# Kernel optimization log

Measured on AMD Instinct MI355X. Metric: run time of the kernel, lower is better.

Reference implementation:

```python
import jax, jax.numpy as jnp
import numpy as np

CROP_H = 7
CROP_W = 7
EXTRAP = 0.0  # module hardcodes 0 when calling CropAndResizeFunction


def _crop_and_resize(image, boxes, box_ind):
    """TF-style crop_and_resize.
    image: (N,C,H,W) float; boxes: (M,4) normalized (y1,x1,y2,x2); box_ind: (M,) int32.
    Returns (M,C,CROP_H,CROP_W).
    """
    N, C, H, W = image.shape
    dt = image.dtype
    y1, x1, y2, x2 = boxes[:, 0], boxes[:, 1], boxes[:, 2], boxes[:, 3]
    ii = jnp.arange(CROP_H, dtype=dt)
    jj = jnp.arange(CROP_W, dtype=dt)
    # sample coordinates in feature-map space, shape (M, CROP_H) / (M, CROP_W)
    y = y1[:, None] * (H - 1) + ii[None, :] * ((y2 - y1) * (H - 1) / (CROP_H - 1))[:, None]
    x = x1[:, None] * (W - 1) + jj[None, :] * ((x2 - x1) * (W - 1) / (CROP_W - 1))[:, None]
    valid_y = (y >= 0) & (y <= H - 1)
    valid_x = (x >= 0) & (x <= W - 1)
    yt_f = jnp.floor(y)
    xt_f = jnp.floor(x)
    y_lerp = y - yt_f  # (M, oh)
    x_lerp = x - xt_f  # (M, ow)
    yt = jnp.clip(yt_f, 0, H - 1).astype(jnp.int32)
    yb = jnp.clip(jnp.ceil(y), 0, H - 1).astype(jnp.int32)
    xl = jnp.clip(xt_f, 0, W - 1).astype(jnp.int32)
    xr = jnp.clip(jnp.ceil(x), 0, W - 1).astype(jnp.int32)
    img = jnp.transpose(image, (0, 2, 3, 1))  # (N,H,W,C) for clean gather
    b = box_ind[:, None, None]                # (M,1,1)
    tl = img[b, yt[:, :, None], xl[:, None, :]]  # (M,oh,ow,C)
    tr = img[b, yt[:, :, None], xr[:, None, :]]
    bl = img[b, yb[:, :, None], xl[:, None, :]]
    br = img[b, yb[:, :, None], xr[:, None, :]]
    xl_w = x_lerp[:, None, :, None]
    top = tl + (tr - tl) * xl_w
    bot = bl + (br - bl) * xl_w
    out = top + (bot - top) * y_lerp[:, :, None, None]
    valid = (valid_y[:, :, None] & valid_x[:, None, :])[..., None]
    out = jnp.where(valid, out, jnp.asarray(EXTRAP, dt))
    return jnp.transpose(out, (0, 3, 1, 2))  # (M,C,oh,ow)


def setup_inputs() -> dict:
    key = jax.random.key(0)
    k0, k1, k2, k3, k4, k5 = jax.random.split(key, 6)
    N, C, H, W = 2, 256, 200, 304
    M = 2048
    scale = 0.0625  # 1/16
    Himg, Wimg = H / scale, W / scale
    featuremap = jax.random.normal(k0, (N, C, H, W), dtype=jnp.float32)
    x1 = jax.random.uniform(k1, (M, 1), minval=0.0, maxval=Wimg - 260.0)
    y1 = jax.random.uniform(k2, (M, 1), minval=0.0, maxval=Himg - 260.0)
    bw = jax.random.uniform(k3, (M, 1), minval=32.0, maxval=256.0)
    bh = jax.random.uniform(k4, (M, 1), minval=32.0, maxval=256.0)
    ids = jax.random.randint(k5, (M, 1), 0, N).astype(jnp.float32)
    rois = jnp.concatenate([ids, x1, y1, x1 + bw, y1 + bh], axis=1)
    return {"featuremap": featuremap, "rois": rois, "spatial_scale": jnp.float32(scale)}


def reference(featuremap, rois, spatial_scale):
    H, W = featuremap.shape[2], featuremap.shape[3]
    boxes = rois[:, 1:5] * spatial_scale
    box_ind = rois[:, 0].astype(jnp.int32)
    x1, y1, x2, y2 = boxes[:, 0], boxes[:, 1], boxes[:, 2], boxes[:, 3]
    spacing_w = (x2 - x1) / CROP_W
    spacing_h = (y2 - y1) / CROP_H
    nx0 = (x1 + spacing_w / 2 - 0.5) / (W - 1)
    ny0 = (y1 + spacing_h / 2 - 0.5) / (H - 1)
    nw = spacing_w * (CROP_W - 1) / (W - 1)
    nh = spacing_h * (CROP_H - 1) / (H - 1)
    boxes_n = jnp.stack([ny0, nx0, ny0 + nh, nx0 + nw], axis=1)
    return _crop_and_resize(featuremap, boxes_n, box_ind)
```

## Files before the change

### kernel.cpp

```cpp
#include <hip/hip_runtime.h>

#define RA_C   256
#define RA_H   200
#define RA_W   304
#define RA_HW  (RA_H * RA_W)
#define RA_CHW (RA_C * RA_HW)
#define CROPN  7
#define CROP2  (CROPN * CROPN)
#define OUT_M  (RA_C * CROP2)
#define BC     16
#define REG_R  16
#define REG_C  20
#define NF4    5
#define CH_STR (REG_R * REG_C + 4)

__global__ __launch_bounds__(256) void roialign_kernel(
    const float* __restrict__ fm, const float* __restrict__ rois,
    const float* __restrict__ scale_p, float* __restrict__ out)
{
    __shared__ __align__(16) float s_reg[BC * CH_STR];
    __shared__ int   s_yt[CROPN], s_yb[CROPN], s_xl[CROPN], s_xr[CROPN];
    __shared__ float s_ylerp[CROPN], s_vy[CROPN], s_xlerp[CROPN], s_vx[CROPN];

    const int t = threadIdx.x;

    const int bid  = blockIdx.x;
    const int numB = gridDim.x >> 4;
    const int xcd  = bid & 7;
    const int rb   = bid >> 3;
    const int cgl  = rb / numB;
    const int m    = rb - cgl * numB;
    const int c0   = (xcd * 2 + cgl) * BC;

    const float scale = scale_p[0];
    const float* __restrict__ rr = rois + (size_t)m * 5;

    if (t < 2 * CROPN) {
        #pragma clang fp contract(off)
        {
            const int axis = (t >= CROPN) ? 1 : 0;
            const int k = axis ? (t - CROPN) : t;
            float lo, hi, szm1;
            if (axis == 0) { lo = rr[2] * scale; hi = rr[4] * scale; szm1 = (float)(RA_H - 1); }
            else           { lo = rr[1] * scale; hi = rr[3] * scale; szm1 = (float)(RA_W - 1); }
            float sp   = (hi - lo) / 7.0f;
            float n0   = (lo + sp * 0.5f - 0.5f) / szm1;
            float nsz  = sp * 6.0f / szm1;
            float b2   = n0 + nsz;
            float d    = (b2 - n0) * szm1 / 6.0f;
            float coord = n0 * szm1 + (float)k * d;
            float fl = floorf(coord);
            float ce = ceilf(coord);
            float lerp = coord - fl;
            int lo_i = (int)fminf(fmaxf(fl, 0.0f), szm1);
            int hi_i = (int)fminf(fmaxf(ce, 0.0f), szm1);
            float valid = (coord >= 0.0f && coord <= szm1) ? 1.0f : 0.0f;
            if (axis == 0) {
                s_yt[k] = lo_i; s_yb[k] = hi_i;
                s_ylerp[k] = lerp; s_vy[k] = valid;
            } else {
                s_xl[k] = lo_i; s_xr[k] = hi_i;
                s_xlerp[k] = lerp; s_vx[k] = valid;
            }
        }
    }

    int ys, xs, base;
    {
        #pragma clang fp contract(off)
        float ylo = rr[2] * scale, yhi = rr[4] * scale;
        float xlo = rr[1] * scale, xhi = rr[3] * scale;
        float spy = (yhi - ylo) / 7.0f;
        float n0y = (ylo + spy * 0.5f - 0.5f) / 199.0f;
        float cy  = n0y * 199.0f;
        float spx = (xhi - xlo) / 7.0f;
        float n0x = (xlo + spx * 0.5f - 0.5f) / 303.0f;
        float cx  = n0x * 303.0f;
        ys = (int)fminf(fmaxf(floorf(cy), 0.0f), 199.0f);
        xs = ((int)fminf(fmaxf(floorf(cx), 0.0f), 303.0f)) & ~3;
        base = (int)rr[0] * RA_CHW + c0 * RA_HW;
    }

    const int cc  = t >> 4;
    const int l16 = t & 15;
    const float* __restrict__ cp = fm + (size_t)(base + cc * RA_HW);
    float4 v[NF4];
    #pragma unroll
    for (int s = 0; s < NF4; ++s) {
        const int idx = l16 + (s << 4);
        const int r2  = idx / 5;
        const int kk  = idx - r2 * 5;
        const int row = min(ys + r2, RA_H - 1);
        const int col = min(xs + (kk << 2), RA_W - 4);
        v[s] = *reinterpret_cast<const float4*>(cp + row * RA_W + col);
    }
    {
        float* __restrict__ sp_ = s_reg + cc * CH_STR;
        #pragma unroll
        for (int s = 0; s < NF4; ++s) {
            const int idx = l16 + (s << 4);
            *reinterpret_cast<float4*>(sp_ + (idx << 2)) = v[s];
        }
    }
    __syncthreads();

    const int ij  = t & 63;
    const int ch4 = t >> 6;
    if (ij < CROP2) {
        const int i = ij / CROPN;
        const int j = ij - i * CROPN;
        const int rT = min(s_yt[i] - ys, REG_R - 1);
        const int rB = min(s_yb[i] - ys, REG_R - 1);
        const int cl = min(s_xl[j] - xs, REG_C - 1);
        const int cr = min(s_xr[j] - xs, REG_C - 1);
        const float yw = s_ylerp[i];
        const float xw = s_xlerp[j];
        const float vv = s_vy[i] * s_vx[j];
        const int oT = rT * REG_C;
        const int oB = rB * REG_C;
        float* __restrict__ op =
            out + (size_t)m * OUT_M + (size_t)(c0 + ch4 * 4) * CROP2 + ij;
        #pragma unroll
        for (int q = 0; q < 4; ++q) {
            const float* __restrict__ sp2 = s_reg + (ch4 * 4 + q) * CH_STR;
            const float tl = sp2[oT + cl];
            const float tr = sp2[oT + cr];
            const float bl = sp2[oB + cl];
            const float br = sp2[oB + cr];
            const float top = tl + (tr - tl) * xw;
            const float bot = bl + (br - bl) * xw;
            op[q * CROP2] = (top + (bot - top) * yw) * vv;
        }
    }
}

extern "C" void kernel_launch(void* const* d_in, const int* in_sizes, int n_in,
                              void* d_out, int out_size, void* d_ws, size_t ws_size,
                              hipStream_t stream) {
    const float* fm    = (const float*)d_in[0];
    const float* rois  = (const float*)d_in[1];
    const float* scale = (const float*)d_in[2];
    float* out = (float*)d_out;
    const int M = in_sizes[1] / 5;
    roialign_kernel<<<dim3(16 * M), dim3(256), 0, stream>>>(fm, rois, scale, out);
}
```

Measured before the change: 292.7 us.

## Process two ROIs per block with 8-channel groups and overlap setup with loads

Each block now handles two ROIs with 8 channels each instead of one ROI with 16 channels, and the channel-group/XCD mapping changes to match. The per-ROI coordinate table is now computed after the global feature loads are issued, so that arithmetic overlaps load latency. Block count and shared memory per block stay the same. The launch assumes M is even, since an odd M would leave the last ROI unprocessed.

```diff
diff --git a/kernel.cpp b/kernel.cpp
--- a/kernel.cpp
+++ b/kernel.cpp
@@ -8,7 +8,8 @@
 #define CROPN  7
 #define CROP2  (CROPN * CROPN)
 #define OUT_M  (RA_C * CROP2)
-#define BC     16
+#define BC     8
+#define BB     2
 #define REG_R  16
 #define REG_C  20
 #define NF4    5
@@ -18,52 +19,26 @@
     const float* __restrict__ fm, const float* __restrict__ rois,
     const float* __restrict__ scale_p, float* __restrict__ out)
 {
-    __shared__ __align__(16) float s_reg[BC * CH_STR];
-    __shared__ int   s_yt[CROPN], s_yb[CROPN], s_xl[CROPN], s_xr[CROPN];
-    __shared__ float s_ylerp[CROPN], s_vy[CROPN], s_xlerp[CROPN], s_vx[CROPN];
+    __shared__ __align__(16) float s_reg[BB * BC * CH_STR];
+    __shared__ int   s_yt[BB][CROPN], s_yb[BB][CROPN];
+    __shared__ int   s_xl[BB][CROPN], s_xr[BB][CROPN];
+    __shared__ float s_ylerp[BB][CROPN], s_vy[BB][CROPN];
+    __shared__ float s_xlerp[BB][CROPN], s_vx[BB][CROPN];
 
     const int t = threadIdx.x;
 
-    const int bid  = blockIdx.x;
-    const int numB = gridDim.x >> 4;
-    const int xcd  = bid & 7;
-    const int rb   = bid >> 3;
-    const int cgl  = rb / numB;
-    const int m    = rb - cgl * numB;
-    const int c0   = (xcd * 2 + cgl) * BC;
+    const int bid   = blockIdx.x;
+    const int numBG = gridDim.x >> 5;
+    const int xcd   = bid & 7;
+    const int r     = bid >> 3;
+    const int cgl   = r / numBG;
+    const int bg    = r - cgl * numBG;
+    const int m0    = bg * BB;
+    const int c0    = (xcd * 4 + cgl) * BC;
 
+    const int bx = t >> 7;
     const float scale = scale_p[0];
-    const float* __restrict__ rr = rois + (size_t)m * 5;
-
-    if (t < 2 * CROPN) {
-        #pragma clang fp contract(off)
-        {
-            const int axis = (t >= CROPN) ? 1 : 0;
-            const int k = axis ? (t - CROPN) : t;
-            float lo, hi, szm1;
-            if (axis == 0) { lo = rr[2] * scale; hi = rr[4] * scale; szm1 = (float)(RA_H - 1); }
-            else           { lo = rr[1] * scale; hi = rr[3] * scale; szm1 = (float)(RA_W - 1); }
-            float sp   = (hi - lo) / 7.0f;
-            float n0   = (lo + sp * 0.5f - 0.5f) / szm1;
-            float nsz  = sp * 6.0f / szm1;
-            float b2   = n0 + nsz;
-            float d    = (b2 - n0) * szm1 / 6.0f;
-            float coord = n0 * szm1 + (float)k * d;
-            float fl = floorf(coord);
-            float ce = ceilf(coord);
-            float lerp = coord - fl;
-            int lo_i = (int)fminf(fmaxf(fl, 0.0f), szm1);
-            int hi_i = (int)fminf(fmaxf(ce, 0.0f), szm1);
-            float valid = (coord >= 0.0f && coord <= szm1) ? 1.0f : 0.0f;
-            if (axis == 0) {
-                s_yt[k] = lo_i; s_yb[k] = hi_i;
-                s_ylerp[k] = lerp; s_vy[k] = valid;
-            } else {
-                s_xl[k] = lo_i; s_xr[k] = hi_i;
-                s_xlerp[k] = lerp; s_vx[k] = valid;
-            }
-        }
-    }
+    const float* __restrict__ rr = rois + (size_t)(m0 + bx) * 5;
 
     int ys, xs, base;
     {
@@ -81,8 +56,9 @@
         base = (int)rr[0] * RA_CHW + c0 * RA_HW;
     }
 
-    const int cc  = t >> 4;
-    const int l16 = t & 15;
+    const int u   = t & 127;
+    const int cc  = u >> 4;
+    const int l16 = u & 15;
     const float* __restrict__ cp = fm + (size_t)(base + cc * RA_HW);
     float4 v[NF4];
     #pragma unroll
@@ -94,8 +70,42 @@
         const int col = min(xs + (kk << 2), RA_W - 4);
         v[s] = *reinterpret_cast<const float4*>(cp + row * RA_W + col);
     }
+
+    if (t < BB * 2 * CROPN) {
+        #pragma clang fp contract(off)
+        {
+            const int mm  = t / (2 * CROPN);
+            const int k14 = t - mm * (2 * CROPN);
+            const int axis = (k14 >= CROPN) ? 1 : 0;
+            const int k = axis ? (k14 - CROPN) : k14;
+            const float* __restrict__ rg = rois + (size_t)(m0 + mm) * 5;
+            float lo, hi, szm1;
+            if (axis == 0) { lo = rg[2] * scale; hi = rg[4] * scale; szm1 = (float)(RA_H - 1); }
+            else           { lo = rg[1] * scale; hi = rg[3] * scale; szm1 = (float)(RA_W - 1); }
+            float sp   = (hi - lo) / 7.0f;
+            float n0   = (lo + sp * 0.5f - 0.5f) / szm1;
+            float nsz  = sp * 6.0f / szm1;
+            float b2   = n0 + nsz;
+            float d    = (b2 - n0) * szm1 / 6.0f;
+            float coord = n0 * szm1 + (float)k * d;
+            float fl = floorf(coord);
+            float ce = ceilf(coord);
+            float lerp = coord - fl;
+            int lo_i = (int)fminf(fmaxf(fl, 0.0f), szm1);
+            int hi_i = (int)fminf(fmaxf(ce, 0.0f), szm1);
+            float valid = (coord >= 0.0f && coord <= szm1) ? 1.0f : 0.0f;
+            if (axis == 0) {
+                s_yt[mm][k] = lo_i; s_yb[mm][k] = hi_i;
+                s_ylerp[mm][k] = lerp; s_vy[mm][k] = valid;
+            } else {
+                s_xl[mm][k] = lo_i; s_xr[mm][k] = hi_i;
+                s_xlerp[mm][k] = lerp; s_vx[mm][k] = valid;
+            }
+        }
+    }
+
     {
-        float* __restrict__ sp_ = s_reg + cc * CH_STR;
+        float* __restrict__ sp_ = s_reg + (bx * BC + cc) * CH_STR;
         #pragma unroll
         for (int s = 0; s < NF4; ++s) {
             const int idx = l16 + (s << 4);
@@ -105,24 +115,25 @@
     __syncthreads();
 
     const int ij  = t & 63;
-    const int ch4 = t >> 6;
+    const int chg = (t >> 6) & 1;
     if (ij < CROP2) {
         const int i = ij / CROPN;
         const int j = ij - i * CROPN;
-        const int rT = min(s_yt[i] - ys, REG_R - 1);
-        const int rB = min(s_yb[i] - ys, REG_R - 1);
-        const int cl = min(s_xl[j] - xs, REG_C - 1);
-        const int cr = min(s_xr[j] - xs, REG_C - 1);
-        const float yw = s_ylerp[i];
-        const float xw = s_xlerp[j];
-        const float vv = s_vy[i] * s_vx[j];
+        const int rT = min(s_yt[bx][i] - ys, REG_R - 1);
+        const int rB = min(s_yb[bx][i] - ys, REG_R - 1);
+        const int cl = min(s_xl[bx][j] - xs, REG_C - 1);
+        const int cr = min(s_xr[bx][j] - xs, REG_C - 1);
+        const float yw = s_ylerp[bx][i];
+        const float xw = s_xlerp[bx][j];
+        const float vv = s_vy[bx][i] * s_vx[bx][j];
         const int oT = rT * REG_C;
         const int oB = rB * REG_C;
         float* __restrict__ op =
-            out + (size_t)m * OUT_M + (size_t)(c0 + ch4 * 4) * CROP2 + ij;
+            out + (size_t)(m0 + bx) * OUT_M + (size_t)(c0 + chg * 4) * CROP2 + ij;
         #pragma unroll
         for (int q = 0; q < 4; ++q) {
-            const float* __restrict__ sp2 = s_reg + (ch4 * 4 + q) * CH_STR;
+            const float* __restrict__ sp2 =
+                s_reg + (bx * BC + chg * 4 + q) * CH_STR;
             const float tl = sp2[oT + cl];
             const float tr = sp2[oT + cr];
             const float bl = sp2[oB + cl];
@@ -142,5 +153,6 @@
     const float* scale = (const float*)d_in[2];
     float* out = (float*)d_out;
     const int M = in_sizes[1] / 5;
-    roialign_kernel<<<dim3(16 * M), dim3(256), 0, stream>>>(fm, rois, scale, out);
+    const int numBG = M / BB;
+    roialign_kernel<<<dim3(32 * numBG), dim3(256), 0, stream>>>(fm, rois, scale, out);
 }
```

New measurement: 268.4 us. -8.3%, faster.
